# Optimization experiments

Hardware: AMD Instinct MI355X
Metric: run time of the kernel (lower is better)

Reference implementation:

```python
import jax, jax.numpy as jnp
import numpy as np

NUM_HEADS = 4
KEY_DIM = 128


def rel_to_abs(rel):
    # rel: [B, heads, L, ww, 2*ww-1] -> [B, heads, L, ww, ww]
    B, heads, L, ww, dim = rel.shape
    flat = rel.reshape(B, heads, L, ww * (2 * ww - 1))[:, :, :, ww - 1:-1]
    return flat.reshape(B, heads, L, ww, 2 * (ww - 1))[..., :ww]


def relative_logits(pos_q, pos_emb_w, pos_emb_h):
    # pos_q: [B, hh, ww, heads, kd]
    # width logits
    q_w = jnp.transpose(pos_q, (0, 3, 1, 2, 4))           # [B, heads, hh, ww, kd]
    rel_w = jnp.einsum('bhxyd,dr->bhxyr', q_w, pos_emb_w)  # [B, heads, hh, ww, 2ww-1]
    rel_w = rel_to_abs(rel_w)                              # [B, heads, hh, ww, ww]
    # height logits
    q_h = jnp.transpose(pos_q, (0, 3, 2, 1, 4))           # [B, heads, ww, hh, kd]
    rel_h = jnp.einsum('bhyxd,dr->bhyxr', q_h, pos_emb_h)  # [B, heads, ww, hh, 2hh-1]
    rel_h = rel_to_abs(rel_h)                              # [B, heads, ww, hh, hh]
    rel_h = jnp.transpose(rel_h, (0, 1, 3, 2, 4))          # [B, heads, hh, ww, hh]
    # broadcast-add: [B, heads, hh, ww, hh, ww]
    return rel_w[:, :, :, :, None, :] + rel_h[:, :, :, :, :, None]


def setup_inputs() -> dict:
    key = jax.random.key(0)
    ks = jax.random.split(key, 7)
    B, H, W, C = 8, 32, 32, 512
    emb = NUM_HEADS * KEY_DIM
    stddev = KEY_DIM ** (-0.5)
    return {
        'x': jax.random.normal(ks[0], (B, H, W, C), jnp.float32),
        'Wq': jax.random.normal(ks[1], (C, emb), jnp.float32) * 0.02,
        'Wk': jax.random.normal(ks[2], (C, emb), jnp.float32) * 0.02,
        'Wv': jax.random.normal(ks[3], (C, emb), jnp.float32) * 0.02,
        'Wo': jax.random.normal(ks[4], (emb, emb), jnp.float32) * 0.02,
        'pos_emb_w': jax.random.normal(ks[5], (KEY_DIM, 2 * W - 1), jnp.float32) * stddev,
        'pos_emb_h': jax.random.normal(ks[6], (KEY_DIM, 2 * H - 1), jnp.float32) * stddev,
    }


def reference(x, Wq, Wk, Wv, Wo, pos_emb_w, pos_emb_h):
    B, hh, ww, C = x.shape
    heads, kd = NUM_HEADS, KEY_DIM
    L = hh * ww
    scale = 1.0 / jnp.sqrt(jnp.asarray(kd, x.dtype))

    q = (x @ Wq) * scale                                    # [B, hh, ww, heads*kd]
    attn_q = q.reshape(B, L, heads, kd).transpose(0, 2, 1, 3)   # [B, heads, L, kd]
    pos_q = q.reshape(B, hh, ww, heads, kd)
    k = (x @ Wk).reshape(B, L, heads, kd).transpose(0, 2, 3, 1)  # [B, heads, kd, L]
    v = (x @ Wv).reshape(B, L, heads, kd).transpose(0, 2, 1, 3)  # [B, heads, L, kd]

    scores = attn_q @ k                                      # [B, heads, L, L]
    pos = relative_logits(pos_q, pos_emb_w, pos_emb_h)        # [B, heads, hh, ww, hh, ww]
    scores = scores + pos.reshape(B, heads, L, L)
    attn = jax.nn.softmax(scores, axis=-1)

    out = attn @ v                                            # [B, heads, L, kd]
    out = out.transpose(0, 2, 1, 3).reshape(B, hh, ww, heads * kd)
    return out @ Wo
```

## Files before the change

### kernel.cpp

```cpp
#include <hip/hip_runtime.h>
#include <math.h>

typedef unsigned short u16;
typedef unsigned int u32;
typedef __bf16 bf16x8 __attribute__((ext_vector_type(8)));
typedef float f32x4 __attribute__((ext_vector_type(4)));

__device__ __forceinline__ u16 f2b(float f) {
  u32 u = __builtin_bit_cast(u32, f);
  u32 r = (u + 0x7FFFu + ((u >> 16) & 1u)) >> 16;
  return (u16)r;
}

__device__ __forceinline__ float b2f(u16 b) {
  u32 u = ((u32)b) << 16;
  return __builtin_bit_cast(float, u);
}

__device__ __forceinline__ void glds16(const void* g, void* lds) {
  __builtin_amdgcn_global_load_lds(
      (const __attribute__((address_space(1))) void*)(void*)(const_cast<void*>(g)),
      (__attribute__((address_space(3))) void*)lds, 16, 0, 0);
}


__global__ __launch_bounds__(256) void castx(const float* __restrict__ x, u16* __restrict__ xb) {
  int idx = blockIdx.x * 256 + threadIdx.x;
  float4 v = ((const float4*)x)[idx];
  ushort4 o;
  o.x = f2b(v.x); o.y = f2b(v.y); o.z = f2b(v.z); o.w = f2b(v.w);
  ((ushort4*)xb)[idx] = o;
}

__global__ __launch_bounds__(256) void buildw(const float* __restrict__ Wq, const float* __restrict__ Wk,
                                              const float* __restrict__ Wv, const float* __restrict__ Wo,
                                              u16* __restrict__ WbigT, u16* __restrict__ WoT) {
  const float SCALE = 0.08838834764831845f;
  int row = blockIdx.x;
  int t = threadIdx.x;
  if (row < 512) {
    for (int k = t; k < 512; k += 256) WbigT[row*512 + k] = f2b(Wq[k*512 + row] * SCALE);
  } else if (row < 1024) {
    int n = row - 512;
    for (int k = t; k < 512; k += 256) WbigT[row*512 + k] = f2b(Wk[k*512 + n]);
  } else if (row < 1536) {
    int n = row - 1024;
    for (int k = t; k < 512; k += 256) WbigT[row*512 + k] = f2b(Wv[k*512 + n]);
  } else if (row < 1544) {
    int rr = row - 1536 + 2040;
    for (int k = t; k < 512; k += 256) WbigT[rr*512 + k] = 0;
  } else {
    int n = row - 1544;
    for (int k = t; k < 512; k += 256) WoT[n*512 + k] = f2b(Wo[k*512 + n]);
  }
}

__global__ __launch_bounds__(256) void wpe_kernel(const float* __restrict__ Wq, const float* __restrict__ pew,
                                                  const float* __restrict__ peh, u16* __restrict__ WbigT) {
  int k = blockIdx.x;
  int t = threadIdx.x;
  __shared__ float wrow[512];
  for (int j = t; j < 512; j += 256) wrow[j] = Wq[k*512 + j];
  __syncthreads();
  if (t < 252) {
    int h = t / 63, r = t - h*63;
    float aw = 0.f, ah = 0.f;
    for (int d = 0; d < 128; d++) {
      float qv = wrow[h*128 + d];
      aw += qv * pew[d*63 + r];
      ah += qv * peh[d*63 + r];
    }
    const float SCALE = 0.08838834764831845f;
    WbigT[(size_t)(1536 + t)*512 + k] = f2b(aw * SCALE);
    WbigT[(size_t)(1788 + t)*512 + k] = f2b(ah * SCALE);
  }
}

__global__ __launch_bounds__(512) void gemm256(
    const u16* __restrict__ A, const u16* __restrict__ Bt,
    u16* __restrict__ Qb, u16* __restrict__ Kb, u16* __restrict__ Vt,
    float* __restrict__ RELW, float* __restrict__ RELH)
{
  __shared__ char sm[131072];
  const int tid = threadIdx.x;
  const int w = tid >> 6, l = tid & 63, g = l >> 4, c = l & 15;
  const int bm = blockIdx.x, bn = blockIdx.y;
  const int wm = w >> 2, wn = w & 3;

  f32x4 acc[8][4];
#pragma unroll
  for (int i = 0; i < 8; i++)
#pragma unroll
    for (int j = 0; j < 4; j++) acc[i][j] = f32x4{0.f, 0.f, 0.f, 0.f};

  const char* Ab = (const char*)A;
  const char* Bb = (const char*)Bt;
  const int rsub = l >> 3;
  const int csw = (((l & 7) ^ rsub) << 4);

#define G_STAGE(kb, p)                                                                    \
  {                                                                                       \
    char* As_ = sm + (p)*65536;                                                           \
    char* Bs_ = As_ + 32768;                                                              \
    const int kbyte = (kb) * 128;                                                         \
    _Pragma("unroll")                                                                     \
    for (int i2 = 0; i2 < 4; i2++) {                                                      \
      const int row = i2*64 + w*8 + rsub;                                                 \
      glds16(Ab + (size_t)(bm*256 + row) * 1024 + kbyte + csw, As_ + i2*8192 + w*1024);   \
      glds16(Bb + (size_t)(bn*256 + row) * 1024 + kbyte + csw, Bs_ + i2*8192 + w*1024);   \
    }                                                                                     \
  }

  G_STAGE(0, 0);
  G_STAGE(1, 1);

#pragma unroll
  for (int kb = 0; kb < 8; kb++) {
    const int p = kb & 1;
    if (kb < 7) { asm volatile("s_waitcnt vmcnt(8)" ::: "memory"); }
    else        { asm volatile("s_waitcnt vmcnt(0)" ::: "memory"); }
    __builtin_amdgcn_s_barrier();
    const char* As_ = sm + p*65536;
    const char* Bs_ = As_ + 32768;
#pragma unroll
    for (int ks = 0; ks < 2; ks++) {
      const int koff = (ks*64 + g*16) ^ ((c & 7) << 4);
      bf16x8 af[8], bfr[4];
#pragma unroll
      for (int mf = 0; mf < 8; mf++)
        af[mf] = *(const bf16x8*)(As_ + (wm*128 + mf*16 + c)*128 + koff);
#pragma unroll
      for (int nf = 0; nf < 4; nf++)
        bfr[nf] = *(const bf16x8*)(Bs_ + (wn*64 + nf*16 + c)*128 + koff);
#pragma unroll
      for (int mf = 0; mf < 8; mf++)
#pragma unroll
        for (int nf = 0; nf < 4; nf++)
          acc[mf][nf] = __builtin_amdgcn_mfma_f32_16x16x32_bf16(af[mf], bfr[nf], acc[mf][nf], 0, 0, 0);
    }
    __builtin_amdgcn_s_barrier();
    if (kb < 6) G_STAGE(kb + 2, p);
  }
#undef G_STAGE

  const int b = bm >> 2;
  const int iBase = (bm & 3) * 256;

  if (bn < 4) {
    u16* dst0 = (bn < 2) ? Qb : Kb;
    const int bnn = bn & 1;
#pragma unroll
    for (int mf = 0; mf < 8; mf++) {
      const int lmb = wm*128 + mf*16 + g*4;
#pragma unroll
      for (int nf = 0; nf < 4; nf++) {
        const int ln = wn*64 + nf*16 + c;
#pragma unroll
        for (int r = 0; r < 4; r++) {
          const int lm = lmb + r;
          *(u16*)(sm + lm*512 + ((ln*2) ^ ((lm & 7) << 4))) = f2b(acc[mf][nf][r]);
        }
      }
    }
    __builtin_amdgcn_s_barrier();
#pragma unroll
    for (int it = 0; it < 16; it++) {
      const int gid = it*512 + tid;
      const int lm2 = gid >> 5, gsub = gid & 31;
      bf16x8 v = *(const bf16x8*)(sm + lm2*512 + ((gsub*16) ^ ((lm2 & 7) << 4)));
      const int h = bnn*2 + (gsub >> 4);
      const int d0 = (gsub & 15) * 8;
      *(bf16x8*)(dst0 + ((size_t)(b*4 + h)*1024 + iBase + lm2)*128 + d0) = v;
    }
  } else if (bn < 6) {
#pragma unroll
    for (int mf = 0; mf < 8; mf++) {
      const int lmb = wm*128 + mf*16 + g*4;
#pragma unroll
      for (int nf = 0; nf < 4; nf++) {
        const int ln = wn*64 + nf*16 + c;
        u32 w0, w1;
        asm("v_cvt_pk_bf16_f32 %0, %1, %2" : "=v"(w0) : "v"(acc[mf][nf][0]), "v"(acc[mf][nf][1]));
        asm("v_cvt_pk_bf16_f32 %0, %1, %2" : "=v"(w1) : "v"(acc[mf][nf][2]), "v"(acc[mf][nf][3]));
        uint2 pk; pk.x = w0; pk.y = w1;
        *(uint2*)(sm + ln*512 + ((lmb*2) ^ ((c & 7) << 4))) = pk;
      }
    }
    __builtin_amdgcn_s_barrier();
#pragma unroll
    for (int it = 0; it < 16; it++) {
      const int gid = it*512 + tid;
      const int ln2 = gid >> 5, gsub = gid & 31;
      bf16x8 v = *(const bf16x8*)(sm + ln2*512 + ((gsub*16) ^ ((ln2 & 7) << 4)));
      const int q2 = (bn - 4)*256 + ln2;
      const int h = q2 >> 7, d = q2 & 127;
      *(bf16x8*)(Vt + ((size_t)(b*4 + h)*128 + d)*1024 + iBase + gsub*8) = v;
    }
  } else {
#pragma unroll
    for (int mf = 0; mf < 8; mf++) {
      const int lmb = wm*128 + mf*16 + g*4;
#pragma unroll
      for (int nf = 0; nf < 4; nf++) {
        const int q = (bn - 6)*256 + wn*64 + nf*16 + c;
        if (q < 252) {
          const int h = q / 63, r2 = q - h*63;
#pragma unroll
          for (int r = 0; r < 4; r++)
            RELW[(size_t)((b*4 + h)*1024 + iBase + lmb + r)*64 + r2] = acc[mf][nf][r];
        } else if (q < 504) {
          const int qq = q - 252;
          const int h = qq / 63, r2 = qq - h*63;
#pragma unroll
          for (int r = 0; r < 4; r++)
            RELH[(size_t)((b*4 + h)*1024 + iBase + lmb + r)*64 + r2] = acc[mf][nf][r];
        }
      }
    }
  }
}

__global__ __launch_bounds__(256) void attn_split(
    const u16* __restrict__ Qb, const u16* __restrict__ Kb, const u16* __restrict__ Vt,
    const float* __restrict__ RELW, const float* __restrict__ RELH,
    u16* __restrict__ Opart, float2* __restrict__ ML)
{
  __shared__ char sm[40960];
  char* const Pl = sm + 32768;
  const int tid = threadIdx.x;
  const int w = tid >> 6, l = tid & 63, g = l >> 4, c = l & 15;
  const int bh = blockIdx.x;
  const int qt = blockIdx.y & 15, half = blockIdx.y >> 4;
  const int i0 = qt * 64, jt0 = half * 8;

  bf16x8 qf[4];
  {
    const char* qbase = (const char*)Qb + (size_t)(bh*1024 + i0 + w*16 + c) * 256;
#pragma unroll
    for (int s = 0; s < 4; s++) qf[s] = *(const bf16x8*)(qbase + s*64 + g*16);
  }

  const int i = i0 + w*16 + c;
  const int xi = i & 31, yi = i >> 5;
  const float* rw = RELW + ((size_t)(bh*1024 + i) << 6);
  const float* rhb = RELH + ((size_t)(bh*1024 + i) << 6) + (31 - yi);
  float xwh[2][4];
#pragma unroll
  for (int e = 0; e < 2; e++)
#pragma unroll
    for (int r = 0; r < 4; r++) xwh[e][r] = rw[e*16 + g*4 + r - xi + 31];

  f32x4 Oacc[8];
#pragma unroll
  for (int fd = 0; fd < 8; fd++) Oacc[fd] = f32x4{0.f, 0.f, 0.f, 0.f};
  float m_q = -INFINITY, l_q = 0.f;

#define KV_STAGE(jt)                                                                       \
  {                                                                                        \
    char* Kt_ = sm;                                                                        \
    char* Vs_ = sm + 16384;                                                                \
    const int j0b = (jt) * 64;                                                             \
    _Pragma("unroll")                                                                      \
    for (int t = 0; t < 4; t++) {                                                          \
      const int L = (w*4 + t)*1024 + l*16;                                                 \
      const int jr = L >> 8, jb = L & 255;                                                 \
      glds16((const char*)Kb + (size_t)(bh*1024 + j0b + jr) * 256 + (jb ^ ((jr & 7) << 4)),\
             Kt_ + L);                                                                     \
      const int dr = L >> 7, db = L & 127;                                                 \
      glds16((const char*)Vt + (size_t)(bh*128 + dr) * 2048 + j0b*2 + (db ^ ((dr & 7) << 4)),\
             Vs_ + L);                                                                     \
    }                                                                                      \
  }

  for (int jj = 0; jj < 8; jj++) {
    const int jt = jt0 + jj;
    const float yh0 = rhb[jt*2], yh1 = rhb[jt*2 + 1];
    KV_STAGE(jt);
    asm volatile("s_waitcnt vmcnt(0)" ::: "memory");
    __builtin_amdgcn_s_barrier();

    const char* Kt_ = sm;
    const char* Vs_ = sm + 16384;

    f32x4 acc[4];
#pragma unroll
    for (int fn = 0; fn < 4; fn++) acc[fn] = f32x4{0.f, 0.f, 0.f, 0.f};
    __builtin_amdgcn_s_setprio(1);
#pragma unroll
    for (int s = 0; s < 4; s++) {
      const int koff = (s*64 + g*16) ^ ((c & 7) << 4);
#pragma unroll
      for (int fn = 0; fn < 4; fn++) {
        bf16x8 kf = *(const bf16x8*)(Kt_ + (fn*16 + c)*256 + koff);
        acc[fn] = __builtin_amdgcn_mfma_f32_16x16x32_bf16(kf, qf[s], acc[fn], 0, 0, 0);
      }
    }
    __builtin_amdgcn_s_setprio(0);

#pragma unroll
    for (int fn = 0; fn < 4; fn++)
#pragma unroll
      for (int r = 0; r < 4; r++)
        acc[fn][r] += xwh[fn & 1][r] + ((fn >> 1) ? yh1 : yh0);

    float mx = fmaxf(fmaxf(fmaxf(acc[0][0], acc[0][1]), fmaxf(acc[0][2], acc[0][3])),
                     fmaxf(fmaxf(acc[1][0], acc[1][1]), fmaxf(acc[1][2], acc[1][3])));
    mx = fmaxf(mx, fmaxf(fmaxf(fmaxf(acc[2][0], acc[2][1]), fmaxf(acc[2][2], acc[2][3])),
                         fmaxf(fmaxf(acc[3][0], acc[3][1]), fmaxf(acc[3][2], acc[3][3]))));
    mx = fmaxf(mx, __shfl_xor(mx, 16));
    mx = fmaxf(mx, __shfl_xor(mx, 32));
    const float mnew = fmaxf(m_q, mx);
    const float scq = __expf(m_q - mnew);
    m_q = mnew;

    float pv[4][4];
    float ps = 0.f;
#pragma unroll
    for (int fn = 0; fn < 4; fn++) {
#pragma unroll
      for (int r = 0; r < 4; r++) {
        pv[fn][r] = __expf(acc[fn][r] - mnew);
        ps += pv[fn][r];
      }
    }
    ps += __shfl_xor(ps, 16);
    ps += __shfl_xor(ps, 32);
    l_q = l_q * scq + ps;

    {
      char* pb = Pl + w*2048 + c*128;
      const int swz = (c & 7) << 4;
#pragma unroll
      for (int fn = 0; fn < 4; fn++) {
        u32 w0, w1;
        asm("v_cvt_pk_bf16_f32 %0, %1, %2" : "=v"(w0) : "v"(pv[fn][0]), "v"(pv[fn][1]));
        asm("v_cvt_pk_bf16_f32 %0, %1, %2" : "=v"(w1) : "v"(pv[fn][2]), "v"(pv[fn][3]));
        uint2 pk; pk.x = w0; pk.y = w1;
        *(uint2*)(pb + ((fn*32 + g*8) ^ swz)) = pk;
      }
    }

#pragma unroll
    for (int r = 0; r < 4; r++) {
      const float scr = __shfl(scq, g*4 + r, 16);
#pragma unroll
      for (int fd = 0; fd < 8; fd++) Oacc[fd][r] *= scr;
    }

    __builtin_amdgcn_s_setprio(1);
#pragma unroll
    for (int s = 0; s < 2; s++) {
      const int koff = (s*64 + g*16) ^ ((c & 7) << 4);
      bf16x8 pf = *(const bf16x8*)(Pl + w*2048 + c*128 + koff);
#pragma unroll
      for (int fd = 0; fd < 8; fd++) {
        bf16x8 vf = *(const bf16x8*)(Vs_ + (fd*16 + c)*128 + koff);
        Oacc[fd] = __builtin_amdgcn_mfma_f32_16x16x32_bf16(pf, vf, Oacc[fd], 0, 0, 0);
      }
    }
    __builtin_amdgcn_s_setprio(0);

    __builtin_amdgcn_s_barrier();
  }
#undef KV_STAGE

  const size_t rbase = (size_t)(half*32 + bh)*1024;
#pragma unroll
  for (int fd = 0; fd < 8; fd++) {
#pragma unroll
    for (int r = 0; r < 4; r++) {
      const int io = i0 + w*16 + g*4 + r;
      Opart[(rbase + io)*128 + fd*16 + c] = f2b(Oacc[fd][r]);
    }
  }
  if (l < 16) {
    float2 s2; s2.x = m_q; s2.y = l_q;
    ML[rbase + i0 + w*16 + l] = s2;
  }
}

__global__ __launch_bounds__(256) void attn_merge(
    u16* __restrict__ Opart, const float2* __restrict__ ML)
{
  const int bh = blockIdx.x, qb = blockIdx.y;
  const int t = threadIdx.x;
  const int row = t >> 3, dg = t & 7;
  const int i = qb*32 + row;
  const size_t r0 = (size_t)bh*1024 + i;
  const size_t r1 = (size_t)(32 + bh)*1024 + i;
  const float2 ml0 = ML[r0], ml1 = ML[r1];
  const float m = fmaxf(ml0.x, ml1.x);
  const float w0 = __expf(ml0.x - m), w1 = __expf(ml1.x - m);
  const float linv = 1.0f / (ml0.y*w0 + ml1.y*w1);
  u16* p0 = Opart + r0*128 + dg*16;
  const u16* p1 = Opart + r1*128 + dg*16;
#pragma unroll
  for (int hlf = 0; hlf < 2; hlf++) {
    bf16x8 a = *(const bf16x8*)(p0 + hlf*8);
    bf16x8 b = *(const bf16x8*)(p1 + hlf*8);
    u16 outv[8];
#pragma unroll
    for (int e = 0; e < 8; e++) {
      float va = b2f(((const u16*)&a)[e]);
      float vb = b2f(((const u16*)&b)[e]);
      outv[e] = f2b((va*w0 + vb*w1) * linv);
    }
    *(bf16x8*)(p0 + hlf*8) = *(const bf16x8*)outv;
  }
}

__global__ __launch_bounds__(256) void gemm_out(
    const u16* __restrict__ A, const u16* __restrict__ Bt, float* __restrict__ outF)
{
  __shared__ char sm[65536];
  const int tid = threadIdx.x;
  const int w = tid >> 6, l = tid & 63, g = l >> 4, c = l & 15;
  const int bm = blockIdx.x, bn = blockIdx.y;
  const int wm = (w >> 1) * 64, wn = (w & 1) * 64;

  f32x4 acc[4][4];
#pragma unroll
  for (int i = 0; i < 4; i++)
#pragma unroll
    for (int j = 0; j < 4; j++) acc[i][j] = f32x4{0.f, 0.f, 0.f, 0.f};

  const char* Ab = (const char*)A;
  const char* Bb = (const char*)Bt;
  const int rsub = l >> 3;
  const int csw = (((l & 7) ^ rsub) << 4);
  const int b_ = bm >> 3;
  const int iT = (bm & 7) * 128;

#define G_STAGE(kb, p)                                                                    \
  {                                                                                       \
    char* As_ = sm + (p)*32768;                                                           \
    char* Bs_ = As_ + 16384;                                                              \
    const int h_ = (kb) >> 1;                                                             \
    const int dof = ((kb) & 1) * 128;                                                     \
    _Pragma("unroll")                                                                     \
    for (int t = 0; t < 4; t++) {                                                         \
      const int row = (w*4 + t)*8 + rsub;                                                 \
      glds16(Ab + (size_t)((b_*4 + h_)*1024 + iT + row) * 256 + dof + csw,                \
             As_ + (w*4 + t)*1024);                                                       \
      glds16(Bb + (size_t)(bn*128 + row) * 1024 + (kb)*128 + csw, Bs_ + (w*4 + t)*1024);  \
    }                                                                                     \
  }

  G_STAGE(0, 0);
  G_STAGE(1, 1);

#pragma unroll
  for (int kb = 0; kb < 8; kb++) {
    const int p = kb & 1;
    if (kb < 7) { asm volatile("s_waitcnt vmcnt(8)" ::: "memory"); }
    else        { asm volatile("s_waitcnt vmcnt(0)" ::: "memory"); }
    __builtin_amdgcn_s_barrier();
    const char* As_ = sm + p*32768;
    const char* Bs_ = As_ + 16384;
#pragma unroll
    for (int ks = 0; ks < 2; ks++) {
      const int koff = (ks*64 + g*16) ^ ((c & 7) << 4);
      bf16x8 af[4], bfr[4];
#pragma unroll
      for (int mf = 0; mf < 4; mf++)
        af[mf] = *(const bf16x8*)(As_ + (wm + mf*16 + c)*128 + koff);
#pragma unroll
      for (int nf = 0; nf < 4; nf++)
        bfr[nf] = *(const bf16x8*)(Bs_ + (wn + nf*16 + c)*128 + koff);
#pragma unroll
      for (int mf = 0; mf < 4; mf++)
#pragma unroll
        for (int nf = 0; nf < 4; nf++)
          acc[mf][nf] = __builtin_amdgcn_mfma_f32_16x16x32_bf16(af[mf], bfr[nf], acc[mf][nf], 0, 0, 0);
    }
    __builtin_amdgcn_s_barrier();
    if (kb < 6) G_STAGE(kb + 2, p);
  }
#undef G_STAGE

#pragma unroll
  for (int mf = 0; mf < 4; mf++) {
#pragma unroll
    for (int nf = 0; nf < 4; nf++) {
      const int n = bn*128 + wn + nf*16 + c;
#pragma unroll
      for (int r = 0; r < 4; r++) {
        const int m = bm*128 + wm + mf*16 + g*4 + r;
        outF[(size_t)m*512 + n] = acc[mf][nf][r];
      }
    }
  }
}

extern "C" void kernel_launch(void* const* d_in, const int* in_sizes, int n_in,
                              void* d_out, int out_size, void* d_ws, size_t ws_size,
                              hipStream_t stream) {
  const float* x   = (const float*)d_in[0];
  const float* Wq  = (const float*)d_in[1];
  const float* Wk  = (const float*)d_in[2];
  const float* Wv  = (const float*)d_in[3];
  const float* Wo  = (const float*)d_in[4];
  const float* pew = (const float*)d_in[5];
  const float* peh = (const float*)d_in[6];

  char* ws = (char*)d_ws;
  u16* xb    = (u16*)ws;    ws += (size_t)8192*512*2;
  u16* WbigT = (u16*)ws;    ws += (size_t)2048*512*2;
  u16* WoT   = (u16*)ws;    ws += (size_t)512*512*2;
  u16* Qb    = (u16*)ws;    ws += (size_t)32*1024*128*2;
  u16* Kb    = (u16*)ws;    ws += (size_t)32*1024*128*2;
  u16* Vt    = (u16*)ws;    ws += (size_t)32*1024*128*2;
  float* RELW = (float*)ws; ws += (size_t)32*1024*64*4;
  float* RELH = (float*)ws; ws += (size_t)32*1024*64*4;
  u16* Opart = (u16*)ws;    ws += (size_t)2*32*1024*128*2;
  float2* MLb = (float2*)ws; ws += (size_t)2*32*1024*8;

  castx<<<4096, 256, 0, stream>>>(x, xb);
  buildw<<<2056, 256, 0, stream>>>(Wq, Wk, Wv, Wo, WbigT, WoT);
  wpe_kernel<<<512, 256, 0, stream>>>(Wq, pew, peh, WbigT);
  gemm256<<<dim3(32, 8), 512, 0, stream>>>(xb, WbigT, Qb, Kb, Vt, RELW, RELH);
  attn_split<<<dim3(32, 32), 256, 0, stream>>>(Qb, Kb, Vt, RELW, RELH, Opart, MLb);
  attn_merge<<<dim3(32, 32), 256, 0, stream>>>(Opart, MLb);
  gemm_out<<<dim3(64, 4), 256, 0, stream>>>(Opart, WoT, (float*)d_out);
}
```

Before: 106.2 us.

## Double-buffer attention KV tiles, fold log2e into Q scale, split GEMM staging

The attention kernel now walks 32-key tiles through a two-slot LDS buffer, prefetching the next tile while computing the current one, where before it used one 64-key buffer that was waited on synchronously. Log2e is folded into the Q and positional weight scale so softmax can use exp2f. The running-max rescale of the output accumulators is skipped unless the new max exceeds the old one by more than 8 (lazy rescaling). The QKV GEMM splits A and B staging so A and B prefetches sit between two MFMA halves, with raised priority, aiming to overlap loads and compute better; the risks are a rarer rescale path and more barriers per tile.

Result: slower. 112.5 us (+5.9%).

```diff
diff --git a/kernel.cpp b/kernel.cpp
--- a/kernel.cpp
+++ b/kernel.cpp
@@ -22,6 +22,8 @@
       (const __attribute__((address_space(1))) void*)(void*)(const_cast<void*>(g)),
       (__attribute__((address_space(3))) void*)lds, 16, 0, 0);
 }
+
+#define QSCALE (0.08838834764831845f * 1.4426950408889634f)
 
 
 __global__ __launch_bounds__(256) void castx(const float* __restrict__ x, u16* __restrict__ xb) {
@@ -35,11 +37,10 @@
 __global__ __launch_bounds__(256) void buildw(const float* __restrict__ Wq, const float* __restrict__ Wk,
                                               const float* __restrict__ Wv, const float* __restrict__ Wo,
                                               u16* __restrict__ WbigT, u16* __restrict__ WoT) {
-  const float SCALE = 0.08838834764831845f;
   int row = blockIdx.x;
   int t = threadIdx.x;
   if (row < 512) {
-    for (int k = t; k < 512; k += 256) WbigT[row*512 + k] = f2b(Wq[k*512 + row] * SCALE);
+    for (int k = t; k < 512; k += 256) WbigT[row*512 + k] = f2b(Wq[k*512 + row] * QSCALE);
   } else if (row < 1024) {
     int n = row - 512;
     for (int k = t; k < 512; k += 256) WbigT[row*512 + k] = f2b(Wk[k*512 + n]);
@@ -70,9 +71,8 @@
       aw += qv * pew[d*63 + r];
       ah += qv * peh[d*63 + r];
     }
-    const float SCALE = 0.08838834764831845f;
-    WbigT[(size_t)(1536 + t)*512 + k] = f2b(aw * SCALE);
-    WbigT[(size_t)(1788 + t)*512 + k] = f2b(ah * SCALE);
+    WbigT[(size_t)(1536 + t)*512 + k] = f2b(aw * QSCALE);
+    WbigT[(size_t)(1788 + t)*512 + k] = f2b(ah * QSCALE);
   }
 }
 
@@ -98,50 +98,85 @@
   const int rsub = l >> 3;
   const int csw = (((l & 7) ^ rsub) << 4);
 
-#define G_STAGE(kb, p)                                                                    \
+#define A_STAGE(kb, p)                                                                    \
   {                                                                                       \
     char* As_ = sm + (p)*65536;                                                           \
-    char* Bs_ = As_ + 32768;                                                              \
     const int kbyte = (kb) * 128;                                                         \
     _Pragma("unroll")                                                                     \
     for (int i2 = 0; i2 < 4; i2++) {                                                      \
       const int row = i2*64 + w*8 + rsub;                                                 \
       glds16(Ab + (size_t)(bm*256 + row) * 1024 + kbyte + csw, As_ + i2*8192 + w*1024);   \
+    }                                                                                     \
+  }
+#define B_STAGE(kb, p)                                                                    \
+  {                                                                                       \
+    char* Bs_ = sm + (p)*65536 + 32768;                                                   \
+    const int kbyte = (kb) * 128;                                                         \
+    _Pragma("unroll")                                                                     \
+    for (int i2 = 0; i2 < 4; i2++) {                                                      \
+      const int row = i2*64 + w*8 + rsub;                                                 \
       glds16(Bb + (size_t)(bn*256 + row) * 1024 + kbyte + csw, Bs_ + i2*8192 + w*1024);   \
     }                                                                                     \
   }
 
-  G_STAGE(0, 0);
-  G_STAGE(1, 1);
+  B_STAGE(0, 0); A_STAGE(0, 0);
+  B_STAGE(1, 1); A_STAGE(1, 1);
 
 #pragma unroll
   for (int kb = 0; kb < 8; kb++) {
     const int p = kb & 1;
-    if (kb < 7) { asm volatile("s_waitcnt vmcnt(8)" ::: "memory"); }
-    else        { asm volatile("s_waitcnt vmcnt(0)" ::: "memory"); }
-    __builtin_amdgcn_s_barrier();
+    if (kb == 0)      { asm volatile("s_waitcnt vmcnt(8)" ::: "memory"); }
+    else if (kb < 7)  { asm volatile("s_waitcnt vmcnt(4)" ::: "memory"); }
+    else              { asm volatile("s_waitcnt vmcnt(0)" ::: "memory"); }
+    __builtin_amdgcn_s_barrier();
+
     const char* As_ = sm + p*65536;
     const char* Bs_ = As_ + 32768;
+
+    bf16x8 bf[4][2], af[4][2];
 #pragma unroll
     for (int ks = 0; ks < 2; ks++) {
       const int koff = (ks*64 + g*16) ^ ((c & 7) << 4);
-      bf16x8 af[8], bfr[4];
-#pragma unroll
-      for (int mf = 0; mf < 8; mf++)
-        af[mf] = *(const bf16x8*)(As_ + (wm*128 + mf*16 + c)*128 + koff);
+#pragma unroll
+      for (int mf = 0; mf < 4; mf++)
+        af[mf][ks] = *(const bf16x8*)(As_ + (wm*128 + mf*16 + c)*128 + koff);
 #pragma unroll
       for (int nf = 0; nf < 4; nf++)
-        bfr[nf] = *(const bf16x8*)(Bs_ + (wn*64 + nf*16 + c)*128 + koff);
-#pragma unroll
-      for (int mf = 0; mf < 8; mf++)
+        bf[nf][ks] = *(const bf16x8*)(Bs_ + (wn*64 + nf*16 + c)*128 + koff);
+    }
+    if (kb >= 1 && kb < 7) A_STAGE(kb + 1, p ^ 1);
+    __builtin_amdgcn_s_setprio(1);
+#pragma unroll
+    for (int ks = 0; ks < 2; ks++)
+#pragma unroll
+      for (int mf = 0; mf < 4; mf++)
 #pragma unroll
         for (int nf = 0; nf < 4; nf++)
-          acc[mf][nf] = __builtin_amdgcn_mfma_f32_16x16x32_bf16(af[mf], bfr[nf], acc[mf][nf], 0, 0, 0);
-    }
-    __builtin_amdgcn_s_barrier();
-    if (kb < 6) G_STAGE(kb + 2, p);
-  }
-#undef G_STAGE
+          acc[mf][nf] = __builtin_amdgcn_mfma_f32_16x16x32_bf16(af[mf][ks], bf[nf][ks], acc[mf][nf], 0, 0, 0);
+    __builtin_amdgcn_s_setprio(0);
+    __builtin_amdgcn_s_barrier();
+
+#pragma unroll
+    for (int ks = 0; ks < 2; ks++) {
+      const int koff = (ks*64 + g*16) ^ ((c & 7) << 4);
+#pragma unroll
+      for (int mf = 0; mf < 4; mf++)
+        af[mf][ks] = *(const bf16x8*)(As_ + (wm*128 + (mf + 4)*16 + c)*128 + koff);
+    }
+    if (kb < 6) B_STAGE(kb + 2, p);
+    __builtin_amdgcn_s_setprio(1);
+#pragma unroll
+    for (int ks = 0; ks < 2; ks++)
+#pragma unroll
+      for (int mf = 0; mf < 4; mf++)
+#pragma unroll
+        for (int nf = 0; nf < 4; nf++)
+          acc[mf + 4][nf] = __builtin_amdgcn_mfma_f32_16x16x32_bf16(af[mf][ks], bf[nf][ks], acc[mf + 4][nf], 0, 0, 0);
+    __builtin_amdgcn_s_setprio(0);
+    __builtin_amdgcn_s_barrier();
+  }
+#undef A_STAGE
+#undef B_STAGE
 
   const int b = bm >> 2;
   const int iBase = (bm & 3) * 256;
@@ -225,13 +260,14 @@
     const float* __restrict__ RELW, const float* __restrict__ RELH,
     u16* __restrict__ Opart, float2* __restrict__ ML)
 {
-  __shared__ char sm[40960];
+  __shared__ char sm[36864];
   char* const Pl = sm + 32768;
   const int tid = threadIdx.x;
   const int w = tid >> 6, l = tid & 63, g = l >> 4, c = l & 15;
   const int bh = blockIdx.x;
   const int qt = blockIdx.y & 15, half = blockIdx.y >> 4;
-  const int i0 = qt * 64, jt0 = half * 8;
+  const int i0 = qt * 64;
+  const int jtg0 = half * 16;
 
   bf16x8 qf[4];
   {
@@ -250,47 +286,53 @@
 #pragma unroll
     for (int r = 0; r < 4; r++) xwh[e][r] = rw[e*16 + g*4 + r - xi + 31];
 
+  float yh = rhb[jtg0];
+  asm volatile("" ::: "memory");
+
+#define KV_STAGE(jtg, p)                                                                    \
+  {                                                                                         \
+    char* Kt_ = sm + (p)*8192;                                                              \
+    char* Vs_ = sm + 16384 + (p)*8192;                                                      \
+    _Pragma("unroll")                                                                       \
+    for (int t = 0; t < 2; t++) {                                                           \
+      const int L = (w*2 + t)*1024 + l*16;                                                  \
+      const int jr = L >> 8, jb = L & 255;                                                  \
+      glds16((const char*)Kb + (size_t)(bh*1024 + (jtg)*32 + jr)*256 + (jb ^ ((jr & 7) << 4)),\
+             Kt_ + L);                                                                      \
+      const int dr = L >> 6, db = L & 63;                                                   \
+      glds16((const char*)Vt + (size_t)(bh*128 + dr)*2048 + (size_t)(jtg)*64 + (db ^ ((dr & 3) << 4)),\
+             Vs_ + L);                                                                      \
+    }                                                                                       \
+  }
+
+  KV_STAGE(jtg0, 0);
+  KV_STAGE(jtg0 + 1, 1);
+
   f32x4 Oacc[8];
 #pragma unroll
   for (int fd = 0; fd < 8; fd++) Oacc[fd] = f32x4{0.f, 0.f, 0.f, 0.f};
   float m_q = -INFINITY, l_q = 0.f;
 
-#define KV_STAGE(jt)                                                                       \
-  {                                                                                        \
-    char* Kt_ = sm;                                                                        \
-    char* Vs_ = sm + 16384;                                                                \
-    const int j0b = (jt) * 64;                                                             \
-    _Pragma("unroll")                                                                      \
-    for (int t = 0; t < 4; t++) {                                                          \
-      const int L = (w*4 + t)*1024 + l*16;                                                 \
-      const int jr = L >> 8, jb = L & 255;                                                 \
-      glds16((const char*)Kb + (size_t)(bh*1024 + j0b + jr) * 256 + (jb ^ ((jr & 7) << 4)),\
-             Kt_ + L);                                                                     \
-      const int dr = L >> 7, db = L & 127;                                                 \
-      glds16((const char*)Vt + (size_t)(bh*128 + dr) * 2048 + j0b*2 + (db ^ ((dr & 7) << 4)),\
-             Vs_ + L);                                                                     \
-    }                                                                                      \
-  }
-
-  for (int jj = 0; jj < 8; jj++) {
-    const int jt = jt0 + jj;
-    const float yh0 = rhb[jt*2], yh1 = rhb[jt*2 + 1];
-    KV_STAGE(jt);
-    asm volatile("s_waitcnt vmcnt(0)" ::: "memory");
-    __builtin_amdgcn_s_barrier();
-
-    const char* Kt_ = sm;
-    const char* Vs_ = sm + 16384;
-
-    f32x4 acc[4];
-#pragma unroll
-    for (int fn = 0; fn < 4; fn++) acc[fn] = f32x4{0.f, 0.f, 0.f, 0.f};
+#pragma unroll 2
+  for (int jj = 0; jj < 16; jj++) {
+    const int jtg = jtg0 + jj;
+    const int p = jj & 1;
+    if (jj < 15) { asm volatile("s_waitcnt vmcnt(4)" ::: "memory"); }
+    else         { asm volatile("s_waitcnt vmcnt(0)" ::: "memory"); }
+    __builtin_amdgcn_s_barrier();
+
+    const char* Kt_ = sm + p*8192;
+    const char* Vs_ = sm + 16384 + p*8192;
+
+    f32x4 acc[2];
+    acc[0] = f32x4{0.f, 0.f, 0.f, 0.f};
+    acc[1] = f32x4{0.f, 0.f, 0.f, 0.f};
     __builtin_amdgcn_s_setprio(1);
 #pragma unroll
     for (int s = 0; s < 4; s++) {
       const int koff = (s*64 + g*16) ^ ((c & 7) << 4);
 #pragma unroll
-      for (int fn = 0; fn < 4; fn++) {
+      for (int fn = 0; fn < 2; fn++) {
         bf16x8 kf = *(const bf16x8*)(Kt_ + (fn*16 + c)*256 + koff);
         acc[fn] = __builtin_amdgcn_mfma_f32_16x16x32_bf16(kf, qf[s], acc[fn], 0, 0, 0);
       }
@@ -298,40 +340,51 @@
     __builtin_amdgcn_s_setprio(0);
 
 #pragma unroll
-    for (int fn = 0; fn < 4; fn++)
+    for (int fn = 0; fn < 2; fn++)
 #pragma unroll
       for (int r = 0; r < 4; r++)
-        acc[fn][r] += xwh[fn & 1][r] + ((fn >> 1) ? yh1 : yh0);
+        acc[fn][r] += xwh[fn][r] + yh;
 
     float mx = fmaxf(fmaxf(fmaxf(acc[0][0], acc[0][1]), fmaxf(acc[0][2], acc[0][3])),
                      fmaxf(fmaxf(acc[1][0], acc[1][1]), fmaxf(acc[1][2], acc[1][3])));
-    mx = fmaxf(mx, fmaxf(fmaxf(fmaxf(acc[2][0], acc[2][1]), fmaxf(acc[2][2], acc[2][3])),
-                         fmaxf(fmaxf(acc[3][0], acc[3][1]), fmaxf(acc[3][2], acc[3][3]))));
     mx = fmaxf(mx, __shfl_xor(mx, 16));
     mx = fmaxf(mx, __shfl_xor(mx, 32));
-    const float mnew = fmaxf(m_q, mx);
-    const float scq = __expf(m_q - mnew);
-    m_q = mnew;
-
-    float pv[4][4];
+
+    if (__any(mx > m_q + 8.f)) {
+      const float mnew = fmaxf(m_q, mx);
+      const float scq = exp2f(m_q - mnew);
+      m_q = mnew;
+      l_q *= scq;
+#pragma unroll
+      for (int r = 0; r < 4; r++) {
+        const float scr = __shfl(scq, g*4 + r, 16);
+#pragma unroll
+        for (int fd = 0; fd < 8; fd++) Oacc[fd][r] *= scr;
+      }
+    }
+
+    float pv[2][4];
     float ps = 0.f;
 #pragma unroll
-    for (int fn = 0; fn < 4; fn++) {
+    for (int fn = 0; fn < 2; fn++) {
 #pragma unroll
       for (int r = 0; r < 4; r++) {
-        pv[fn][r] = __expf(acc[fn][r] - mnew);
+        pv[fn][r] = exp2f(acc[fn][r] - m_q);
         ps += pv[fn][r];
       }
     }
     ps += __shfl_xor(ps, 16);
     ps += __shfl_xor(ps, 32);
-    l_q = l_q * scq + ps;
+    l_q += ps;
+
+    float nyh = 0.f;
+    if (jj < 15) nyh = rhb[jtg + 1];
 
     {
-      char* pb = Pl + w*2048 + c*128;
-      const int swz = (c & 7) << 4;
-#pragma unroll
-      for (int fn = 0; fn < 4; fn++) {
+      char* pb = Pl + w*1024 + c*64;
+      const int swz = (c & 3) << 4;
+#pragma unroll
+      for (int fn = 0; fn < 2; fn++) {
         u32 w0, w1;
         asm("v_cvt_pk_bf16_f32 %0, %1, %2" : "=v"(w0) : "v"(pv[fn][0]), "v"(pv[fn][1]));
         asm("v_cvt_pk_bf16_f32 %0, %1, %2" : "=v"(w1) : "v"(pv[fn][2]), "v"(pv[fn][3]));
@@ -340,27 +393,20 @@
       }
     }
 
-#pragma unroll
-    for (int r = 0; r < 4; r++) {
-      const float scr = __shfl(scq, g*4 + r, 16);
-#pragma unroll
-      for (int fd = 0; fd < 8; fd++) Oacc[fd][r] *= scr;
-    }
-
     __builtin_amdgcn_s_setprio(1);
-#pragma unroll
-    for (int s = 0; s < 2; s++) {
-      const int koff = (s*64 + g*16) ^ ((c & 7) << 4);
-      bf16x8 pf = *(const bf16x8*)(Pl + w*2048 + c*128 + koff);
+    {
+      bf16x8 pf = *(const bf16x8*)(Pl + w*1024 + c*64 + ((g*16) ^ ((c & 3) << 4)));
 #pragma unroll
       for (int fd = 0; fd < 8; fd++) {
-        bf16x8 vf = *(const bf16x8*)(Vs_ + (fd*16 + c)*128 + koff);
+        bf16x8 vf = *(const bf16x8*)(Vs_ + (fd*16 + c)*64 + ((g*16) ^ ((c & 3) << 4)));
         Oacc[fd] = __builtin_amdgcn_mfma_f32_16x16x32_bf16(pf, vf, Oacc[fd], 0, 0, 0);
       }
     }
     __builtin_amdgcn_s_setprio(0);
 
     __builtin_amdgcn_s_barrier();
+    if (jj < 14) KV_STAGE(jtg + 2, p);
+    yh = nyh;
   }
 #undef KV_STAGE
 
@@ -390,7 +436,7 @@
   const size_t r1 = (size_t)(32 + bh)*1024 + i;
   const float2 ml0 = ML[r0], ml1 = ML[r1];
   const float m = fmaxf(ml0.x, ml1.x);
-  const float w0 = __expf(ml0.x - m), w1 = __expf(ml1.x - m);
+  const float w0 = exp2f(ml0.x - m), w1 = exp2f(ml1.x - m);
   const float linv = 1.0f / (ml0.y*w0 + ml1.y*w1);
   u16* p0 = Opart + r0*128 + dg*16;
   const u16* p1 = Opart + r1*128 + dg*16;
```
